# Performance work log

Measured on AMD Instinct MI355X. Metric: run time of the kernel, lower is better.

The kernel has to match this reference:

```python
import jax, jax.numpy as jnp
import numpy as np

N_NODES = 100000
N_EDGES = 3200000
F_IN = 256
D_OUT = 64
BATCH = 4096
N_FIELDS = 20


def setup_inputs() -> dict:
    key = jax.random.key(0)
    k1, k2, k3, k4 = jax.random.split(key, 4)
    features = jax.random.normal(k1, (N_NODES, F_IN), dtype=jnp.float32)
    edge_index = jax.random.randint(k2, (2, N_EDGES), 0, N_NODES, dtype=jnp.int32)
    W = jax.random.normal(k3, (F_IN, D_OUT), dtype=jnp.float32) * 0.05
    b = jnp.zeros((D_OUT,), dtype=jnp.float32)
    x = jax.random.randint(k4, (BATCH, N_FIELDS), 0, N_NODES, dtype=jnp.int32)
    return {"features": features, "edge_index": edge_index, "W": W, "b": b, "x": x}


def reference(features, edge_index, W, b, x):
    # PyG GCNConv: add self-loops, symmetric normalization, linear transform,
    # scatter-add aggregation, then final index by x.
    n = features.shape[0]
    loop = jnp.arange(n, dtype=edge_index.dtype)
    src = jnp.concatenate([edge_index[0], loop])  # [E+N]
    dst = jnp.concatenate([edge_index[1], loop])
    ones = jnp.ones(src.shape[0], dtype=features.dtype)
    deg = jax.ops.segment_sum(ones, dst, num_segments=n)  # in-degree incl. self-loop
    deg_inv_sqrt = jnp.where(deg > 0, jax.lax.rsqrt(deg), 0.0)
    norm = deg_inv_sqrt[src] * deg_inv_sqrt[dst]  # [E+N]
    xw = features @ W  # [N, D] -- transform before aggregation (fewer FLOPs)
    msg = xw[src] * norm[:, None]  # gather + scale
    out = jax.ops.segment_sum(msg, dst, num_segments=n) + b  # [N, D]
    return out[x]  # [batch, num_fields, D]
```

## Files before the change

kernel.cpp:

```cpp
#include <hip/hip_runtime.h>
#include <hip/hip_bf16.h>

#define N_NODES 100000
#define N_EDGES 3200000
#define F_IN 256
#define D_OUT 64
#define BATCH 4096
#define N_FIELDS 20
#define N_ENTRIES (BATCH * N_FIELDS)

#define NBUCKET 512
#define NPB 196
#define N_PAD (NBUCKET * NPB)
#define EPB 8192
#define NBLK ((N_EDGES + EPB - 1) / EPB)
#define BUCKET_CAP 8192
#define SCAN_B 512
#define NSB (N_PAD / SCAN_B)
#define CNT_BLKS (N_ENTRIES / 256)
#define WT_BLKS (D_OUT * F_IN / 256)

typedef short bf16x8 __attribute__((ext_vector_type(8)));
typedef float f32x4 __attribute__((ext_vector_type(4)));

static __device__ __forceinline__ unsigned short f2bf_bits(float x) {
    __hip_bfloat16 h = __float2bfloat16(x);
    return *reinterpret_cast<unsigned short*>(&h);
}

__global__ __launch_bounds__(256) void k_front(const uint4* __restrict__ dst4,
                                               unsigned short* __restrict__ perBlockCnt,
                                               const int* __restrict__ x,
                                               int* __restrict__ nodeEntCnt,
                                               unsigned* __restrict__ refBits,
                                               const float* __restrict__ W,
                                               unsigned short* __restrict__ WTbf) {
    if (blockIdx.x < NBLK) {
        __shared__ unsigned hist[NBUCKET];
        hist[threadIdx.x] = 0;
        hist[threadIdx.x + 256] = 0;
        __syncthreads();
        int base4 = blockIdx.x * (EPB / 4);
#pragma unroll
        for (int k = 0; k < EPB / 1024; k++) {
            int e4 = base4 + k * 256 + threadIdx.x;
            if (e4 < N_EDGES / 4) {
                uint4 d = dst4[e4];
                atomicAdd(&hist[d.x / NPB], 1u);
                atomicAdd(&hist[d.y / NPB], 1u);
                atomicAdd(&hist[d.z / NPB], 1u);
                atomicAdd(&hist[d.w / NPB], 1u);
            }
        }
        __syncthreads();
        perBlockCnt[(threadIdx.x) * NBLK + blockIdx.x] = (unsigned short)hist[threadIdx.x];
        perBlockCnt[(threadIdx.x + 256) * NBLK + blockIdx.x] = (unsigned short)hist[threadIdx.x + 256];
    } else if (blockIdx.x < NBLK + CNT_BLKS) {
        int ent = (blockIdx.x - NBLK) * 256 + threadIdx.x;
        if (ent < N_ENTRIES) {
            int node = x[ent];
            atomicAdd(&nodeEntCnt[node], 1);
            atomicOr(&refBits[node >> 5], 1u << (node & 31));
        }
    } else {
        int i = (blockIdx.x - NBLK - CNT_BLKS) * 256 + threadIdx.x;
        if (i < D_OUT * F_IN) {
            int n = i >> 8, k = i & 255;
            WTbf[i] = f2bf_bits(W[k * D_OUT + n]);
        }
    }
}

__global__ __launch_bounds__(512) void k_scans(const int* __restrict__ nodeEntCnt,
                                               int* __restrict__ localE,
                                               int* __restrict__ blockSumsE,
                                               unsigned short* __restrict__ perBlockCnt,
                                               int* __restrict__ bucketTot) {
    if (blockIdx.x < NSB) {
        __shared__ int sh[SCAN_B];
        int g = blockIdx.x * SCAN_B + threadIdx.x;
        int v = (g < N_PAD) ? nodeEntCnt[g] : 0;
        sh[threadIdx.x] = v;
        __syncthreads();
        for (int off = 1; off < SCAN_B; off <<= 1) {
            int t = (threadIdx.x >= off) ? sh[threadIdx.x - off] : 0;
            __syncthreads();
            sh[threadIdx.x] += t;
            __syncthreads();
        }
        int incl = sh[threadIdx.x];
        if (g < N_PAD) localE[g] = incl - v;
        if (threadIdx.x == SCAN_B - 1) blockSumsE[blockIdx.x] = incl;
    } else {
        int gw = ((blockIdx.x - NSB) * 512 + threadIdx.x) >> 6;
        int lane = threadIdx.x & 63;
        if (gw >= NBUCKET) return;
        unsigned running = 0;
        for (int c = 0; c < (NBLK + 63) / 64; c++) {
            int blk = c * 64 + lane;
            int idx = gw * NBLK + blk;
            unsigned v = (blk < NBLK) ? perBlockCnt[idx] : 0;
            unsigned orig = v;
#pragma unroll
            for (int d = 1; d < 64; d <<= 1) {
                unsigned t = __shfl_up(v, d, 64);
                if (lane >= d) v += t;
            }
            if (blk < NBLK) perBlockCnt[idx] = (unsigned short)(running + v - orig);
            running += __shfl(v, 63, 64);
        }
        if (lane == 0) bucketTot[gw] = (int)running;
    }
}

__global__ __launch_bounds__(512) void k_base2(const int* __restrict__ bucketTot,
                                               int* __restrict__ bucketBase,
                                               const int* __restrict__ blockSumsE,
                                               int* __restrict__ blockBaseE) {
    __shared__ int sh[512];
    int tid = threadIdx.x;
    if (blockIdx.x == 0) {
        int v = bucketTot[tid];
        sh[tid] = v;
        __syncthreads();
        for (int off = 1; off < 512; off <<= 1) {
            int t = (tid >= off) ? sh[tid - off] : 0;
            __syncthreads();
            sh[tid] += t;
            __syncthreads();
        }
        bucketBase[tid] = sh[tid] - v;
        if (tid == NBUCKET - 1) bucketBase[NBUCKET] = sh[NBUCKET - 1];
    } else {
        int v = (tid < NSB) ? blockSumsE[tid] : 0;
        sh[tid] = v;
        __syncthreads();
        for (int off = 1; off < 512; off <<= 1) {
            int t = (tid >= off) ? sh[tid - off] : 0;
            __syncthreads();
            sh[tid] += t;
            __syncthreads();
        }
        if (tid < NSB) blockBaseE[tid] = sh[tid] - v;
    }
}

__global__ __launch_bounds__(256) void k_scatters(const uint4* __restrict__ src4,
                                                  const uint4* __restrict__ dst4,
                                                  const int* __restrict__ bucketBase,
                                                  const unsigned short* __restrict__ perBlockCnt,
                                                  unsigned* __restrict__ bucketData,
                                                  const int* __restrict__ x,
                                                  int* __restrict__ localE,
                                                  const int* __restrict__ blockBaseE,
                                                  int* __restrict__ entGrouped) {
    if (blockIdx.x < NBLK) {
        __shared__ unsigned slotBase[NBUCKET];
        slotBase[threadIdx.x] = (unsigned)bucketBase[threadIdx.x] +
                                (unsigned)perBlockCnt[threadIdx.x * NBLK + blockIdx.x];
        slotBase[threadIdx.x + 256] = (unsigned)bucketBase[threadIdx.x + 256] +
                                      (unsigned)perBlockCnt[(threadIdx.x + 256) * NBLK + blockIdx.x];
        __syncthreads();
        int base4 = blockIdx.x * (EPB / 4);
#pragma unroll
        for (int k = 0; k < EPB / 1024; k++) {
            int e4 = base4 + k * 256 + threadIdx.x;
            if (e4 < N_EDGES / 4) {
                uint4 s = src4[e4];
                uint4 d = dst4[e4];
                unsigned ss[4] = {s.x, s.y, s.z, s.w};
                unsigned dd[4] = {d.x, d.y, d.z, d.w};
#pragma unroll
                for (int j = 0; j < 4; j++) {
                    unsigned b = dd[j] / NPB;
                    unsigned ld = dd[j] - b * NPB;
                    unsigned slot = atomicAdd(&slotBase[b], 1u);
                    bucketData[slot] = ss[j] | (ld << 17);
                }
            }
        }
    } else {
        int ent = (blockIdx.x - NBLK) * 256 + threadIdx.x;
        if (ent < N_ENTRIES) {
            int node = x[ent];
            int posL = atomicAdd(&localE[node], 1);
            entGrouped[blockBaseE[node >> 9] + posL] = ent;
        }
    }
}

__global__ __launch_bounds__(256) void k_bucket_csr(unsigned* __restrict__ bucketData,
                                                    const int* __restrict__ bucketBase,
                                                    const unsigned* __restrict__ refBits,
                                                    int* __restrict__ rowStart,
                                                    unsigned short* __restrict__ deg) {
    __shared__ unsigned srcsorted[BUCKET_CAP];
    __shared__ unsigned nodeCount[NPB];
    __shared__ unsigned sscan[256];
    __shared__ unsigned cursor[NPB];
    __shared__ unsigned char refF[NPB];

    int b = blockIdx.x;
    int base = bucketBase[b];
    int cnt = bucketBase[b + 1] - base;
    if (cnt > BUCKET_CAP) cnt = BUCKET_CAP;
    int tid = threadIdx.x;

    for (int j = tid; j < NPB; j += 256) nodeCount[j] = 0;
    __syncthreads();

    for (int i = tid; i < cnt; i += 256) {
        unsigned w = bucketData[base + i];
        atomicAdd(&nodeCount[w >> 17], 1u);
    }
    __syncthreads();

    int firstNode = b * NPB;
    unsigned refCnt = 0;
    if (tid < NPB) {
        int node = firstNode + tid;
        unsigned isRef = (refBits[node >> 5] >> (node & 31)) & 1u;
        refF[tid] = (unsigned char)isRef;
        refCnt = isRef ? nodeCount[tid] : 0;
        deg[node] = (unsigned short)nodeCount[tid];
    }
    sscan[tid] = refCnt;
    __syncthreads();
    for (int off = 1; off < 256; off <<= 1) {
        unsigned t = (tid >= off) ? sscan[tid - off] : 0;
        __syncthreads();
        sscan[tid] += t;
        __syncthreads();
    }

    if (tid < NPB) {
        unsigned excl = sscan[tid] - refCnt;
        rowStart[firstNode + tid] = base + (int)excl;
        cursor[tid] = excl;
    }
    __syncthreads();

    for (int i = tid; i < cnt; i += 256) {
        unsigned w = bucketData[base + i];
        unsigned ld = w >> 17;
        if (refF[ld]) {
            unsigned slot = atomicAdd(&cursor[ld], 1u);
            srcsorted[slot] = w & 0x1FFFFu;
        }
    }
    __syncthreads();

    int refTotal = (int)sscan[255];
    for (int i = tid; i < refTotal; i += 256)
        bucketData[base + i] = srcsorted[i];
}

__global__ __launch_bounds__(256) void k_gemm_mfma(const float* __restrict__ feat,
                                                   const unsigned short* __restrict__ WTbf,
                                                   const unsigned short* __restrict__ deg,
                                                   unsigned short* __restrict__ y) {
    __shared__ unsigned short wt[64 * 264];
    int tid = threadIdx.x;
    {
        int r = tid >> 2, seg = tid & 3;
        const uint4* gsrc = (const uint4*)(WTbf + r * 256 + seg * 64);
        uint4* ldst = (uint4*)&wt[r * 264 + seg * 64];
#pragma unroll
        for (int q = 0; q < 8; q++) ldst[q] = gsrc[q];
    }
    __syncthreads();

    int wave = tid >> 6, lane = tid & 63;
    int quad = lane >> 4, m = lane & 15;
    int rowT = blockIdx.x * 64 + wave * 16;
    int row = rowT + m;
    int rowC = (row < N_NODES) ? row : (N_NODES - 1);
    const float* fb = feat + (size_t)rowC * F_IN + quad * 8;

    f32x4 acc0 = {0.f, 0.f, 0.f, 0.f};
    f32x4 acc1 = acc0, acc2 = acc0, acc3 = acc0;

#pragma unroll
    for (int kk = 0; kk < 8; kk++) {
        float4 x0 = *(const float4*)(fb + kk * 32);
        float4 x1 = *(const float4*)(fb + kk * 32 + 4);
        bf16x8 a;
        a[0] = (short)f2bf_bits(x0.x); a[1] = (short)f2bf_bits(x0.y);
        a[2] = (short)f2bf_bits(x0.z); a[3] = (short)f2bf_bits(x0.w);
        a[4] = (short)f2bf_bits(x1.x); a[5] = (short)f2bf_bits(x1.y);
        a[6] = (short)f2bf_bits(x1.z); a[7] = (short)f2bf_bits(x1.w);
        int kbase = kk * 32 + quad * 8;
        bf16x8 b0 = *(const bf16x8*)&wt[(0 * 16 + m) * 264 + kbase];
        bf16x8 b1 = *(const bf16x8*)&wt[(1 * 16 + m) * 264 + kbase];
        bf16x8 b2 = *(const bf16x8*)&wt[(2 * 16 + m) * 264 + kbase];
        bf16x8 b3 = *(const bf16x8*)&wt[(3 * 16 + m) * 264 + kbase];
        acc0 = __builtin_amdgcn_mfma_f32_16x16x32_bf16(a, b0, acc0, 0, 0, 0);
        acc1 = __builtin_amdgcn_mfma_f32_16x16x32_bf16(a, b1, acc1, 0, 0, 0);
        acc2 = __builtin_amdgcn_mfma_f32_16x16x32_bf16(a, b2, acc2, 0, 0, 0);
        acc3 = __builtin_amdgcn_mfma_f32_16x16x32_bf16(a, b3, acc3, 0, 0, 0);
    }

    float dv[4];
#pragma unroll
    for (int r = 0; r < 4; r++) {
        int rr = rowT + quad * 4 + r;
        dv[r] = rsqrtf((float)(deg[rr] + 1));
    }
#pragma unroll
    for (int r = 0; r < 4; r++) {
        int rr = rowT + quad * 4 + r;
        if (rr < N_NODES) {
            size_t o = (size_t)rr * D_OUT + m;
            y[o]      = f2bf_bits(acc0[r] * dv[r]);
            y[o + 16] = f2bf_bits(acc1[r] * dv[r]);
            y[o + 32] = f2bf_bits(acc2[r] * dv[r]);
            y[o + 48] = f2bf_bits(acc3[r] * dv[r]);
        }
    }
}

static __device__ __forceinline__ void acc4(f32x4& a, uint2 v, float msk) {
    a[0] += msk * __uint_as_float(v.x << 16);
    a[1] += msk * __uint_as_float(v.x & 0xffff0000u);
    a[2] += msk * __uint_as_float(v.y << 16);
    a[3] += msk * __uint_as_float(v.y & 0xffff0000u);
}

__global__ __launch_bounds__(256) void k_agg(const int* __restrict__ entGrouped,
                                             const int* __restrict__ localE,
                                             const int* __restrict__ blockBaseE,
                                             const int* __restrict__ rowStart,
                                             const unsigned short* __restrict__ deg,
                                             const unsigned* __restrict__ sortedSrc,
                                             const unsigned short* __restrict__ y,
                                             const float* __restrict__ b,
                                             float* __restrict__ out) {
    int g = blockIdx.x * blockDim.x + threadIdx.x;
    int i = g >> 6, lane = g & 63;
    if (i >= N_PAD) return;
    int gEnd = blockBaseE[i >> 9] + localE[i];
    int gStart = (i == 0) ? 0 : (blockBaseE[(i - 1) >> 9] + localE[i - 1]);
    int cntEnt = gEnd - gStart;
    if (cntEnt <= 0) return;

    int grp = lane >> 4;
    int m = lane & 15;
    int start = rowStart[i];
    int cnt = deg[i];
    float disI = rsqrtf((float)(cnt + 1));

    uint2 sv = *(const uint2*)(y + ((unsigned)i << 6) + (m << 2));

    f32x4 a0 = {0.f, 0.f, 0.f, 0.f};
    f32x4 a1 = a0, a2 = a0, a3 = a0;

    for (int e = 0; e < cnt; e += 32) {
        int e0 = e + grp,      e1 = e + 4 + grp,  e2 = e + 8 + grp,  e3 = e + 12 + grp;
        int e4 = e + 16 + grp, e5 = e + 20 + grp, e6 = e + 24 + grp, e7 = e + 28 + grp;
        unsigned r0 = (e0 < cnt) ? sortedSrc[start + e0] : (unsigned)i;
        unsigned r1 = (e1 < cnt) ? sortedSrc[start + e1] : (unsigned)i;
        unsigned r2 = (e2 < cnt) ? sortedSrc[start + e2] : (unsigned)i;
        unsigned r3 = (e3 < cnt) ? sortedSrc[start + e3] : (unsigned)i;
        unsigned r4 = (e4 < cnt) ? sortedSrc[start + e4] : (unsigned)i;
        unsigned r5 = (e5 < cnt) ? sortedSrc[start + e5] : (unsigned)i;
        unsigned r6 = (e6 < cnt) ? sortedSrc[start + e6] : (unsigned)i;
        unsigned r7 = (e7 < cnt) ? sortedSrc[start + e7] : (unsigned)i;
        uint2 v0 = *(const uint2*)(y + (r0 << 6) + (m << 2));
        uint2 v1 = *(const uint2*)(y + (r1 << 6) + (m << 2));
        uint2 v2 = *(const uint2*)(y + (r2 << 6) + (m << 2));
        uint2 v3 = *(const uint2*)(y + (r3 << 6) + (m << 2));
        uint2 v4 = *(const uint2*)(y + (r4 << 6) + (m << 2));
        uint2 v5 = *(const uint2*)(y + (r5 << 6) + (m << 2));
        uint2 v6 = *(const uint2*)(y + (r6 << 6) + (m << 2));
        uint2 v7 = *(const uint2*)(y + (r7 << 6) + (m << 2));
        acc4(a0, v0, (e0 < cnt) ? 1.f : 0.f);
        acc4(a1, v1, (e1 < cnt) ? 1.f : 0.f);
        acc4(a2, v2, (e2 < cnt) ? 1.f : 0.f);
        acc4(a3, v3, (e3 < cnt) ? 1.f : 0.f);
        acc4(a0, v4, (e4 < cnt) ? 1.f : 0.f);
        acc4(a1, v5, (e5 < cnt) ? 1.f : 0.f);
        acc4(a2, v6, (e6 < cnt) ? 1.f : 0.f);
        acc4(a3, v7, (e7 < cnt) ? 1.f : 0.f);
    }

    f32x4 s;
#pragma unroll
    for (int c = 0; c < 4; c++) s[c] = (a0[c] + a1[c]) + (a2[c] + a3[c]);
#pragma unroll
    for (int c = 0; c < 4; c++) {
        s[c] += __shfl_xor(s[c], 16, 64);
        s[c] += __shfl_xor(s[c], 32, 64);
    }

    float4 b4 = *(const float4*)(b + (m << 2));
    float4 val;
    val.x = disI * (s[0] + __uint_as_float(sv.x << 16)) + b4.x;
    val.y = disI * (s[1] + __uint_as_float(sv.x & 0xffff0000u)) + b4.y;
    val.z = disI * (s[2] + __uint_as_float(sv.y << 16)) + b4.z;
    val.w = disI * (s[3] + __uint_as_float(sv.y & 0xffff0000u)) + b4.w;

    for (int j = grp; j < cntEnt; j += 4) {
        int ent = entGrouped[gStart + j];
        *(float4*)(out + (size_t)ent * D_OUT + (m << 2)) = val;
    }
}

extern "C" void kernel_launch(void* const* d_in, const int* in_sizes, int n_in,
                              void* d_out, int out_size, void* d_ws, size_t ws_size,
                              hipStream_t stream) {
    const float* feat     = (const float*)d_in[0];
    const int* edge_index = (const int*)d_in[1];
    const float* W        = (const float*)d_in[2];
    const float* bsrc     = (const float*)d_in[3];
    const int* x          = (const int*)d_in[4];
    float* out            = (float*)d_out;

    const uint4* src4 = (const uint4*)edge_index;
    const uint4* dst4 = (const uint4*)(edge_index + N_EDGES);

    char* ws = (char*)d_ws;
    size_t off = 0;
    auto alloc = [&](size_t bytes) {
        size_t o = off;
        off = (off + bytes + 255) & ~(size_t)255;
        return o;
    };
    int* bucketBase = (int*)(ws + alloc((size_t)(NBUCKET + 1) * 4));
    int* bucketTot  = (int*)(ws + alloc((size_t)NBUCKET * 4));
    size_t ecOff = alloc((size_t)N_PAD * 4);
    int* nodeEntCnt = (int*)(ws + ecOff);
    int* entGrouped = (int*)(ws + ecOff);
    unsigned* refBits = (unsigned*)(ws + alloc((size_t)(N_PAD / 8)));
    size_t rsOff = alloc((size_t)N_PAD * 4);
    unsigned short* perBlockCnt = (unsigned short*)(ws + rsOff);
    int* rowStart   = (int*)(ws + rsOff);
    unsigned short* deg = (unsigned short*)(ws + alloc((size_t)N_PAD * 2));
    unsigned short* WTbf = (unsigned short*)(ws + alloc((size_t)D_OUT * F_IN * 2));
    int* localE     = (int*)(ws + alloc((size_t)N_PAD * 4));
    int* blockSumsE = (int*)(ws + alloc((size_t)NSB * 4));
    int* blockBaseE = (int*)(ws + alloc((size_t)NSB * 4));
    unsigned* bucketData = (unsigned*)(ws + alloc((size_t)N_EDGES * 4));
    unsigned short* y = (unsigned short*)(ws + alloc((size_t)N_NODES * D_OUT * 2));
    (void)ws_size; (void)in_sizes; (void)n_in; (void)out_size;

    const int T = 256;
    (void)hipMemsetAsync(nodeEntCnt, 0, (size_t)N_PAD * 4, stream);
    (void)hipMemsetAsync(refBits, 0, (size_t)(N_PAD / 8), stream);
    k_front<<<NBLK + CNT_BLKS + WT_BLKS, T, 0, stream>>>(dst4, perBlockCnt, x, nodeEntCnt,
                                                         refBits, W, WTbf);
    k_scans<<<NSB + 64, 512, 0, stream>>>(nodeEntCnt, localE, blockSumsE, perBlockCnt, bucketTot);
    k_base2<<<2, 512, 0, stream>>>(bucketTot, bucketBase, blockSumsE, blockBaseE);
    k_scatters<<<NBLK + CNT_BLKS, T, 0, stream>>>(src4, dst4, bucketBase, perBlockCnt, bucketData,
                                                  x, localE, blockBaseE, entGrouped);
    k_bucket_csr<<<NBUCKET, T, 0, stream>>>(bucketData, bucketBase, refBits, rowStart, deg);
    k_gemm_mfma<<<(N_NODES + 63) / 64, T, 0, stream>>>(feat, WTbf, deg, y);
    k_agg<<<((size_t)N_PAD * 64 + T - 1) / T, T, 0, stream>>>(
        entGrouped, localE, blockBaseE, rowStart, deg, bucketData, y, bsrc, out);
}
```

Measured before the change: 321.5 us.

## Fuse GEMM into front histogram kernel and apply degree scaling in bucket CSR

Moves the bf16 MFMA feature transform out of its own launch and into the front kernel as extra blocks, so it runs alongside the edge histogram and entry-count work. The GEMM now writes unscaled fp32 results, and the bucket CSR kernel applies the rsqrt(deg) scaling and converts them to bf16 using its per-node counts. W transposition moves to a small separate kernel. EPB is doubled to halve the number of histogram blocks. The trade is an extra fp32 intermediate (about 25 MB written and then read back) and higher shared-memory use in every front block, since the weight tile is declared for all of them.

Result: no change. 318.4 us (-1.0%).

```diff
diff --git a/kernel.cpp b/kernel.cpp
--- a/kernel.cpp
+++ b/kernel.cpp
@@ -12,13 +12,13 @@
 #define NBUCKET 512
 #define NPB 196
 #define N_PAD (NBUCKET * NPB)
-#define EPB 8192
+#define EPB 16384
 #define NBLK ((N_EDGES + EPB - 1) / EPB)
 #define BUCKET_CAP 8192
 #define SCAN_B 512
 #define NSB (N_PAD / SCAN_B)
 #define CNT_BLKS (N_ENTRIES / 256)
-#define WT_BLKS (D_OUT * F_IN / 256)
+#define GEMM_BLKS ((N_NODES + 63) / 64)
 
 typedef short bf16x8 __attribute__((ext_vector_type(8)));
 typedef float f32x4 __attribute__((ext_vector_type(4)));
@@ -26,6 +26,13 @@
 static __device__ __forceinline__ unsigned short f2bf_bits(float x) {
     __hip_bfloat16 h = __float2bfloat16(x);
     return *reinterpret_cast<unsigned short*>(&h);
+}
+
+__global__ void k_wtconv(const float* __restrict__ W, unsigned short* __restrict__ WTbf) {
+    int i = blockIdx.x * blockDim.x + threadIdx.x;
+    if (i >= D_OUT * F_IN) return;
+    int n = i >> 8, k = i & 255;
+    WTbf[i] = f2bf_bits(W[k * D_OUT + n]);
 }
 
 __global__ __launch_bounds__(256) void k_front(const uint4* __restrict__ dst4,
@@ -33,17 +40,21 @@
                                                const int* __restrict__ x,
                                                int* __restrict__ nodeEntCnt,
                                                unsigned* __restrict__ refBits,
-                                               const float* __restrict__ W,
-                                               unsigned short* __restrict__ WTbf) {
+                                               const float* __restrict__ feat,
+                                               const unsigned short* __restrict__ WTbf,
+                                               float* __restrict__ yf) {
+    __shared__ unsigned hist[NBUCKET];
+    __shared__ unsigned short wt[64 * 264];
+    int tid = threadIdx.x;
+
     if (blockIdx.x < NBLK) {
-        __shared__ unsigned hist[NBUCKET];
-        hist[threadIdx.x] = 0;
-        hist[threadIdx.x + 256] = 0;
+        hist[tid] = 0;
+        hist[tid + 256] = 0;
         __syncthreads();
         int base4 = blockIdx.x * (EPB / 4);
 #pragma unroll
         for (int k = 0; k < EPB / 1024; k++) {
-            int e4 = base4 + k * 256 + threadIdx.x;
+            int e4 = base4 + k * 256 + tid;
             if (e4 < N_EDGES / 4) {
                 uint4 d = dst4[e4];
                 atomicAdd(&hist[d.x / NPB], 1u);
@@ -53,20 +64,66 @@
             }
         }
         __syncthreads();
-        perBlockCnt[(threadIdx.x) * NBLK + blockIdx.x] = (unsigned short)hist[threadIdx.x];
-        perBlockCnt[(threadIdx.x + 256) * NBLK + blockIdx.x] = (unsigned short)hist[threadIdx.x + 256];
+        perBlockCnt[(tid) * NBLK + blockIdx.x] = (unsigned short)hist[tid];
+        perBlockCnt[(tid + 256) * NBLK + blockIdx.x] = (unsigned short)hist[tid + 256];
     } else if (blockIdx.x < NBLK + CNT_BLKS) {
-        int ent = (blockIdx.x - NBLK) * 256 + threadIdx.x;
+        int ent = (blockIdx.x - NBLK) * 256 + tid;
         if (ent < N_ENTRIES) {
             int node = x[ent];
             atomicAdd(&nodeEntCnt[node], 1);
             atomicOr(&refBits[node >> 5], 1u << (node & 31));
         }
     } else {
-        int i = (blockIdx.x - NBLK - CNT_BLKS) * 256 + threadIdx.x;
-        if (i < D_OUT * F_IN) {
-            int n = i >> 8, k = i & 255;
-            WTbf[i] = f2bf_bits(W[k * D_OUT + n]);
+        int gb = blockIdx.x - NBLK - CNT_BLKS;
+        {
+            int r = tid >> 2, seg = tid & 3;
+            const uint4* gsrc = (const uint4*)(WTbf + r * 256 + seg * 64);
+            uint4* ldst = (uint4*)&wt[r * 264 + seg * 64];
+#pragma unroll
+            for (int q = 0; q < 8; q++) ldst[q] = gsrc[q];
+        }
+        __syncthreads();
+
+        int wave = tid >> 6, lane = tid & 63;
+        int quad = lane >> 4, m = lane & 15;
+        int rowT = gb * 64 + wave * 16;
+        int row = rowT + m;
+        int rowC = (row < N_NODES) ? row : (N_NODES - 1);
+        const float* fb = feat + (size_t)rowC * F_IN + quad * 8;
+
+        f32x4 acc0 = {0.f, 0.f, 0.f, 0.f};
+        f32x4 acc1 = acc0, acc2 = acc0, acc3 = acc0;
+
+#pragma unroll
+        for (int kk = 0; kk < 8; kk++) {
+            float4 x0 = *(const float4*)(fb + kk * 32);
+            float4 x1 = *(const float4*)(fb + kk * 32 + 4);
+            bf16x8 a;
+            a[0] = (short)f2bf_bits(x0.x); a[1] = (short)f2bf_bits(x0.y);
+            a[2] = (short)f2bf_bits(x0.z); a[3] = (short)f2bf_bits(x0.w);
+            a[4] = (short)f2bf_bits(x1.x); a[5] = (short)f2bf_bits(x1.y);
+            a[6] = (short)f2bf_bits(x1.z); a[7] = (short)f2bf_bits(x1.w);
+            int kbase = kk * 32 + quad * 8;
+            bf16x8 b0 = *(const bf16x8*)&wt[(0 * 16 + m) * 264 + kbase];
+            bf16x8 b1 = *(const bf16x8*)&wt[(1 * 16 + m) * 264 + kbase];
+            bf16x8 b2 = *(const bf16x8*)&wt[(2 * 16 + m) * 264 + kbase];
+            bf16x8 b3 = *(const bf16x8*)&wt[(3 * 16 + m) * 264 + kbase];
+            acc0 = __builtin_amdgcn_mfma_f32_16x16x32_bf16(a, b0, acc0, 0, 0, 0);
+            acc1 = __builtin_amdgcn_mfma_f32_16x16x32_bf16(a, b1, acc1, 0, 0, 0);
+            acc2 = __builtin_amdgcn_mfma_f32_16x16x32_bf16(a, b2, acc2, 0, 0, 0);
+            acc3 = __builtin_amdgcn_mfma_f32_16x16x32_bf16(a, b3, acc3, 0, 0, 0);
+        }
+
+#pragma unroll
+        for (int r = 0; r < 4; r++) {
+            int rr = rowT + quad * 4 + r;
+            if (rr < N_NODES) {
+                size_t o = (size_t)rr * D_OUT + m;
+                yf[o]      = acc0[r];
+                yf[o + 16] = acc1[r];
+                yf[o + 32] = acc2[r];
+                yf[o + 48] = acc3[r];
+            }
         }
     }
 }
@@ -193,7 +250,9 @@
                                                     const int* __restrict__ bucketBase,
                                                     const unsigned* __restrict__ refBits,
                                                     int* __restrict__ rowStart,
-                                                    unsigned short* __restrict__ deg) {
+                                                    unsigned short* __restrict__ deg,
+                                                    const float* __restrict__ yf,
+                                                    unsigned short* __restrict__ y) {
     __shared__ unsigned srcsorted[BUCKET_CAP];
     __shared__ unsigned nodeCount[NPB];
     __shared__ unsigned sscan[256];
@@ -253,68 +312,17 @@
     int refTotal = (int)sscan[255];
     for (int i = tid; i < refTotal; i += 256)
         bucketData[base + i] = srcsorted[i];
-}
-
-__global__ __launch_bounds__(256) void k_gemm_mfma(const float* __restrict__ feat,
-                                                   const unsigned short* __restrict__ WTbf,
-                                                   const unsigned short* __restrict__ deg,
-                                                   unsigned short* __restrict__ y) {
-    __shared__ unsigned short wt[64 * 264];
-    int tid = threadIdx.x;
-    {
-        int r = tid >> 2, seg = tid & 3;
-        const uint4* gsrc = (const uint4*)(WTbf + r * 256 + seg * 64);
-        uint4* ldst = (uint4*)&wt[r * 264 + seg * 64];
-#pragma unroll
-        for (int q = 0; q < 8; q++) ldst[q] = gsrc[q];
-    }
-    __syncthreads();
-
-    int wave = tid >> 6, lane = tid & 63;
-    int quad = lane >> 4, m = lane & 15;
-    int rowT = blockIdx.x * 64 + wave * 16;
-    int row = rowT + m;
-    int rowC = (row < N_NODES) ? row : (N_NODES - 1);
-    const float* fb = feat + (size_t)rowC * F_IN + quad * 8;
-
-    f32x4 acc0 = {0.f, 0.f, 0.f, 0.f};
-    f32x4 acc1 = acc0, acc2 = acc0, acc3 = acc0;
-
-#pragma unroll
-    for (int kk = 0; kk < 8; kk++) {
-        float4 x0 = *(const float4*)(fb + kk * 32);
-        float4 x1 = *(const float4*)(fb + kk * 32 + 4);
-        bf16x8 a;
-        a[0] = (short)f2bf_bits(x0.x); a[1] = (short)f2bf_bits(x0.y);
-        a[2] = (short)f2bf_bits(x0.z); a[3] = (short)f2bf_bits(x0.w);
-        a[4] = (short)f2bf_bits(x1.x); a[5] = (short)f2bf_bits(x1.y);
-        a[6] = (short)f2bf_bits(x1.z); a[7] = (short)f2bf_bits(x1.w);
-        int kbase = kk * 32 + quad * 8;
-        bf16x8 b0 = *(const bf16x8*)&wt[(0 * 16 + m) * 264 + kbase];
-        bf16x8 b1 = *(const bf16x8*)&wt[(1 * 16 + m) * 264 + kbase];
-        bf16x8 b2 = *(const bf16x8*)&wt[(2 * 16 + m) * 264 + kbase];
-        bf16x8 b3 = *(const bf16x8*)&wt[(3 * 16 + m) * 264 + kbase];
-        acc0 = __builtin_amdgcn_mfma_f32_16x16x32_bf16(a, b0, acc0, 0, 0, 0);
-        acc1 = __builtin_amdgcn_mfma_f32_16x16x32_bf16(a, b1, acc1, 0, 0, 0);
-        acc2 = __builtin_amdgcn_mfma_f32_16x16x32_bf16(a, b2, acc2, 0, 0, 0);
-        acc3 = __builtin_amdgcn_mfma_f32_16x16x32_bf16(a, b3, acc3, 0, 0, 0);
-    }
-
-    float dv[4];
-#pragma unroll
-    for (int r = 0; r < 4; r++) {
-        int rr = rowT + quad * 4 + r;
-        dv[r] = rsqrtf((float)(deg[rr] + 1));
-    }
-#pragma unroll
-    for (int r = 0; r < 4; r++) {
-        int rr = rowT + quad * 4 + r;
-        if (rr < N_NODES) {
-            size_t o = (size_t)rr * D_OUT + m;
-            y[o]      = f2bf_bits(acc0[r] * dv[r]);
-            y[o + 16] = f2bf_bits(acc1[r] * dv[r]);
-            y[o + 32] = f2bf_bits(acc2[r] * dv[r]);
-            y[o + 48] = f2bf_bits(acc3[r] * dv[r]);
+
+    for (int idx = tid; idx < NPB * 16; idx += 256) {
+        int j = idx >> 4;
+        int node = firstNode + j;
+        if (node < N_NODES) {
+            float ds = rsqrtf((float)nodeCount[j] + 1.0f);
+            float4 v = ((const float4*)(yf + (size_t)node * D_OUT))[idx & 15];
+            uint2 pw;
+            pw.x = (unsigned)f2bf_bits(v.x * ds) | ((unsigned)f2bf_bits(v.y * ds) << 16);
+            pw.y = (unsigned)f2bf_bits(v.z * ds) | ((unsigned)f2bf_bits(v.w * ds) << 16);
+            ((uint2*)(y + (size_t)node * D_OUT))[idx & 15] = pw;
         }
     }
 }
@@ -441,19 +449,20 @@
     int* blockBaseE = (int*)(ws + alloc((size_t)NSB * 4));
     unsigned* bucketData = (unsigned*)(ws + alloc((size_t)N_EDGES * 4));
     unsigned short* y = (unsigned short*)(ws + alloc((size_t)N_NODES * D_OUT * 2));
+    float* yf       = (float*)(ws + alloc((size_t)N_NODES * D_OUT * 4));
     (void)ws_size; (void)in_sizes; (void)n_in; (void)out_size;
 
     const int T = 256;
     (void)hipMemsetAsync(nodeEntCnt, 0, (size_t)N_PAD * 4, stream);
     (void)hipMemsetAsync(refBits, 0, (size_t)(N_PAD / 8), stream);
-    k_front<<<NBLK + CNT_BLKS + WT_BLKS, T, 0, stream>>>(dst4, perBlockCnt, x, nodeEntCnt,
-                                                         refBits, W, WTbf);
+    k_wtconv<<<(D_OUT * F_IN + T - 1) / T, T, 0, stream>>>(W, WTbf);
+    k_front<<<NBLK + CNT_BLKS + GEMM_BLKS, T, 0, stream>>>(dst4, perBlockCnt, x, nodeEntCnt,
+                                                           refBits, feat, WTbf, yf);
     k_scans<<<NSB + 64, 512, 0, stream>>>(nodeEntCnt, localE, blockSumsE, perBlockCnt, bucketTot);
     k_base2<<<2, 512, 0, stream>>>(bucketTot, bucketBase, blockSumsE, blockBaseE);
     k_scatters<<<NBLK + CNT_BLKS, T, 0, stream>>>(src4, dst4, bucketBase, perBlockCnt, bucketData,
                                                   x, localE, blockBaseE, entGrouped);
-    k_bucket_csr<<<NBUCKET, T, 0, stream>>>(bucketData, bucketBase, refBits, rowStart, deg);
-    k_gemm_mfma<<<(N_NODES + 63) / 64, T, 0, stream>>>(feat, WTbf, deg, y);
+    k_bucket_csr<<<NBUCKET, T, 0, stream>>>(bucketData, bucketBase, refBits, rowStart, deg, yf, y);
     k_agg<<<((size_t)N_PAD * 64 + T - 1) / T, T, 0, stream>>>(
         entGrouped, localE, blockBaseE, rowStart, deg, bucketData, y, bsrc, out);
 }
```
